# Kernel optimization log

Measured on AMD Instinct MI355X. Metric: run time of the kernel, lower is better.

## Reference

```python
import jax, jax.numpy as jnp
import numpy as np

B, N, E = 8, 4096, 8190
V, H, OUT = 256, 128, 128


def setup_inputs() -> dict:
    key = jax.random.key(0)
    ks = jax.random.split(key, 7)
    return {
        "type_ids": jax.random.randint(ks[0], (B, N), 0, V),
        "edges": jax.random.randint(ks[1], (B, E, 2), 0, N),
        "emb": jax.random.normal(ks[2], (V, H), jnp.float32) * 0.02,
        "w1": jax.random.normal(ks[3], (H, H), jnp.float32) * (1.0 / np.sqrt(H)),
        "b1": jax.random.normal(ks[4], (H,), jnp.float32) * 0.01,
        "w2": jax.random.normal(ks[5], (OUT, H), jnp.float32) * (1.0 / np.sqrt(H)),
        "b2": jax.random.normal(ks[6], (OUT,), jnp.float32) * 0.01,
    }


def reference(type_ids, edges, emb, w1, b1, w2, b2):
    # X: [B, N, H] embedded node types
    X = emb[type_ids]
    b_idx = jnp.broadcast_to(jnp.arange(type_ids.shape[0])[:, None], edges.shape[:2])
    # dense adjacency, set (not add) like torch adj[i, j] = 1.0; then + I
    adj = jnp.zeros((type_ids.shape[0], N, N), X.dtype)
    adj = adj.at[b_idx, edges[..., 0], edges[..., 1]].set(1.0)
    adj = adj + jnp.eye(N, dtype=X.dtype)
    # symmetric degree normalization: A = D^-1/2 (adj) D^-1/2
    deg = adj.sum(axis=-1)
    dis = jnp.maximum(deg, 1.0) ** -0.5  # deg.clamp(min=1.0) ** -0.5
    A = dis[:, :, None] * adj * dis[:, None, :]
    # two-layer GCN (torch Linear: x @ W.T + b)
    h = jax.nn.relu(jnp.einsum("bnm,bmh->bnh", A, X) @ w1.T + b1)
    z = jnp.einsum("bnm,bmh->bnh", A, h) @ w2.T + b2
    zbar = z.mean(axis=1)  # per-graph mean pool -> [B, OUT]
    # F.normalize(dim=-1), eps=1e-12
    norm = jnp.maximum(jnp.linalg.norm(zbar, axis=-1, keepdims=True), 1e-12)
    return zbar / norm
```

## Files before the change

kernel.cpp:

```cpp
#include <hip/hip_runtime.h>
#include <hip/hip_bf16.h>
#include <stdint.h>

#define BB 8
#define NN 4096
#define NE 8190
#define VV 256
#define HH 128
#define WPR2 128
#define MAXD 32
#define SLICES 32
#define RPW 4
#define NWAVE (BB * NN / RPW)


__device__ __forceinline__ int deco(int v) {
    unsigned u = (unsigned)v;
    return (int)(u - (u >= 0xAAAAAAAAu ? 0xAAAAAAAAu : 0u));
}

__global__ void k_scatter_embw1(const int* __restrict__ edges,
                                const float* __restrict__ emb,
                                const float* __restrict__ w1,
                                unsigned long long* __restrict__ bits,
                                int2* __restrict__ deg,
                                unsigned short* __restrict__ outl,
                                unsigned short* __restrict__ inl,
                                float* __restrict__ embw1) {
    int blk = blockIdx.x, t = threadIdx.x;
    if (blk < 256) {
        int idx = blk * 256 + t;
        if (idx >= BB * NE) return;
        int b = idx / NE;
        int src = edges[idx * 2 + 0];
        int dst = edges[idx * 2 + 1];
        int row = b * NN + src;
        unsigned long long m = 1ull << (2 * (dst & 31));
        unsigned long long old =
            atomicOr(&bits[(size_t)row * WPR2 + (dst >> 5)], m);
        if (!(old & m)) {
            int po = deco(atomicAdd(&deg[row].x, 1));
            if (po < MAXD) outl[(size_t)row * MAXD + po] = (unsigned short)dst;
            int col = b * NN + dst;
            int pi = deco(atomicAdd(&deg[col].y, 1));
            if (pi < MAXD) inl[(size_t)col * MAXD + pi] = (unsigned short)src;
        }
    } else {
        __shared__ float er[256];
        int v = (blk - 256) * 2 + (t >> 7);
        int o = t & 127;
        er[t] = emb[v * HH + o];
        __syncthreads();
        const float* erow = &er[(t >> 7) * HH];
        float acc = 0.f;
#pragma unroll 8
        for (int k = 0; k < HH; k++) acc += erow[k] * w1[o * HH + k];
        embw1[v * HH + o] = acc;
    }
}

__global__ void __launch_bounds__(256)
k_fused(const int* __restrict__ type_ids,
        const float* __restrict__ embw1,
        const int2* __restrict__ deg,
        const unsigned short* __restrict__ outl,
        const unsigned short* __restrict__ inl,
        const float* __restrict__ b1,
        float* __restrict__ p) {
    int lane = threadIdx.x & 63;
    int wid  = threadIdx.x >> 6;
    int gw   = blockIdx.x * 4 + wid;
    int base = gw * RPW;
    int b    = base >> 12;
    int e    = lane & 31;
    bool isOut = (lane < 32);
    float2 b1v = ((const float2*)b1)[lane];
    float2 psum; psum.x = 0.f; psum.y = 0.f;

    for (int r = 0; r < RPW; r++) {
        int row = base + r;
        int2 dg = deg[row];
        int odeg = deco(dg.x);
        int mo = min(odeg, MAXD);
        int mi = min(deco(dg.y), MAXD);
        int tid_i = type_ids[row];
        float dval = 0.f; int tval = 0;
        if (isOut ? (e < mo) : (e < mi)) {
            const unsigned short* lst = isOut ? outl : inl;
            int gj = b * NN + (int)lst[(size_t)row * MAXD + e];
            dval = rsqrtf((float)(deco(deg[gj].x) + 1));
            if (isOut) tval = type_ids[gj];
        }
        float s = dval;
#pragma unroll
        for (int off = 1; off <= 16; off <<= 1)
            s += __shfl_xor(s, off);
        float s_in = __shfl(s, 32);
        float dis_i = rsqrtf((float)(odeg + 1));
        float c_i = dis_i * (s_in + dis_i);
        float2 ev = ((const float2*)(embw1 + tid_i * HH))[lane];
        float2 acc; acc.x = dis_i * ev.x; acc.y = dis_i * ev.y;
        for (int q = 0; q < mo; q++) {
            float dj = __shfl(dval, q);
            int   tj = __shfl(tval, q);
            float2 evq = ((const float2*)(embw1 + tj * HH))[lane];
            acc.x += dj * evq.x;
            acc.y += dj * evq.y;
        }
        float h0 = fmaxf(dis_i * acc.x + b1v.x, 0.f);
        float h1 = fmaxf(dis_i * acc.y + b1v.y, 0.f);
        psum.x += c_i * h0;
        psum.y += c_i * h1;
    }
    int slice = gw & (SLICES - 1);
    float* pp = &p[((size_t)b * SLICES + slice) * HH + 2 * lane];
    atomicAdd(pp + 0, psum.x);
    atomicAdd(pp + 1, psum.y);
}

__global__ void k_final(const float* __restrict__ p,
                        const float* __restrict__ w2,
                        const float* __restrict__ b2,
                        float* __restrict__ out) {
    __shared__ float pl[HH];
    __shared__ float red[HH];
    int b = blockIdx.x, o = threadIdx.x;
    float accp = 0.f;
#pragma unroll 8
    for (int sct = 0; sct < SLICES; sct++)
        accp += p[((size_t)b * SLICES + sct) * HH + o];
    pl[o] = accp * (1.0f / (float)NN);
    __syncthreads();
    float acc = b2[o];
#pragma unroll 8
    for (int k = 0; k < HH; k++) acc += pl[k] * w2[o * HH + k];
    red[o] = acc * acc;
    __syncthreads();
    for (int stride = 64; stride > 0; stride >>= 1) {
        if (o < stride) red[o] += red[o + stride];
        __syncthreads();
    }
    float denom = fmaxf(sqrtf(red[0]), 1e-12f);
    out[b * HH + o] = acc / denom;
}

extern "C" void kernel_launch(void* const* d_in, const int* in_sizes, int n_in,
                              void* d_out, int out_size, void* d_ws, size_t ws_size,
                              hipStream_t stream) {
    const int*   type_ids = (const int*)d_in[0];
    const int*   edges    = (const int*)d_in[1];
    const float* emb      = (const float*)d_in[2];
    const float* w1       = (const float*)d_in[3];
    const float* b1       = (const float*)d_in[4];
    const float* w2       = (const float*)d_in[5];
    const float* b2       = (const float*)d_in[6];
    float* out = (float*)d_out;

    char* ws = (char*)d_ws;
    unsigned long long* bits = (unsigned long long*)ws;
    size_t off = (size_t)BB * NN * WPR2 * 8;
    int2* deg = (int2*)(ws + off);   off += (size_t)BB * NN * 8;
    float* p  = (float*)(ws + off);  off += (size_t)BB * SLICES * HH * 4;
    unsigned short* outl = (unsigned short*)(ws + off); off += (size_t)BB * NN * MAXD * 2;
    unsigned short* inl  = (unsigned short*)(ws + off); off += (size_t)BB * NN * MAXD * 2;
    float* embw1 = (float*)(ws + off);

    k_scatter_embw1<<<384, 256, 0, stream>>>(edges, emb, w1, bits, deg,
                                             outl, inl, embw1);
    k_fused<<<NWAVE / 4, 256, 0, stream>>>(type_ids, embw1, deg, outl, inl,
                                           b1, p);
    k_final<<<BB, HH, 0, stream>>>(p, w2, b2, out);
}
```

Before: 101.2 us.

## Vectorize loads, batch neighbor gathers, pack degree and type, widen final kernel

Vectorizes edge loads and the emb·W1 dot product with float4 reads. In the fused kernel, loads type ids and degrees for all four rows at once, issues every neighbor-list and degree gather before any compute so the loads overlap, and packs the truncated rsqrt degree and the type id into one int. Each neighbor then costs a single shuffle instead of two. The in-degree sum becomes a serial shuffle loop, and truncating the low mantissa bits slightly lowers precision. k_final uses 256 threads with split reductions, and launch bounds now request higher occupancy.

```diff
diff --git a/kernel.cpp b/kernel.cpp
--- a/kernel.cpp
+++ b/kernel.cpp
@@ -32,8 +32,9 @@
         int idx = blk * 256 + t;
         if (idx >= BB * NE) return;
         int b = idx / NE;
-        int src = edges[idx * 2 + 0];
-        int dst = edges[idx * 2 + 1];
+        int2 ed = ((const int2*)edges)[idx];
+        int src = ed.x;
+        int dst = ed.y;
         int row = b * NN + src;
         unsigned long long m = 1ull << (2 * (dst & 31));
         unsigned long long old =
@@ -51,15 +52,19 @@
         int o = t & 127;
         er[t] = emb[v * HH + o];
         __syncthreads();
-        const float* erow = &er[(t >> 7) * HH];
+        const float4* e4 = (const float4*)&er[(t >> 7) * HH];
+        const float4* w4 = (const float4*)(w1 + o * HH);
         float acc = 0.f;
-#pragma unroll 8
-        for (int k = 0; k < HH; k++) acc += erow[k] * w1[o * HH + k];
+#pragma unroll
+        for (int k = 0; k < HH / 4; k++) {
+            float4 a = e4[k], w = w4[k];
+            acc += a.x * w.x + a.y * w.y + a.z * w.z + a.w * w.w;
+        }
         embw1[v * HH + o] = acc;
     }
 }
 
-__global__ void __launch_bounds__(256)
+__global__ void __launch_bounds__(256, 8)
 k_fused(const int* __restrict__ type_ids,
         const float* __restrict__ embw1,
         const int2* __restrict__ deg,
@@ -72,38 +77,59 @@
     int gw   = blockIdx.x * 4 + wid;
     int base = gw * RPW;
     int b    = base >> 12;
+    int bN   = base & ~(NN - 1);
     int e    = lane & 31;
     bool isOut = (lane < 32);
     float2 b1v = ((const float2*)b1)[lane];
     float2 psum; psum.x = 0.f; psum.y = 0.f;
 
+    int4 t4 = *(const int4*)(type_ids + base);
+    int4 dA = *((const int4*)(deg + base));
+    int4 dB = *((const int4*)(deg + base) + 1);
+    int dgx[RPW] = {dA.x, dA.z, dB.x, dB.z};
+    int dgy[RPW] = {dA.y, dA.w, dB.y, dB.w};
+    int tii[RPW] = {t4.x, t4.y, t4.z, t4.w};
+
+    int nb[RPW];
+#pragma unroll
     for (int r = 0; r < RPW; r++) {
-        int row = base + r;
-        int2 dg = deg[row];
-        int odeg = deco(dg.x);
+        int m = isOut ? min(deco(dgx[r]), MAXD) : min(deco(dgy[r]), MAXD);
+        nb[r] = -1;
+        if (e < m) {
+            const unsigned short* lst = isOut ? outl : inl;
+            nb[r] = (int)lst[(size_t)(base + r) * MAXD + e];
+        }
+    }
+
+    int pk[RPW];
+#pragma unroll
+    for (int r = 0; r < RPW; r++) {
+        int v = 0;
+        if (nb[r] >= 0) {
+            int gj = bN + nb[r];
+            float dv = rsqrtf((float)(deco(deg[gj].x) + 1));
+            int tj = isOut ? type_ids[gj] : 0;
+            v = (__float_as_int(dv) & 0xFFFFFF00) | tj;
+        }
+        pk[r] = v;
+    }
+
+#pragma unroll
+    for (int r = 0; r < RPW; r++) {
+        int odeg = deco(dgx[r]);
         int mo = min(odeg, MAXD);
-        int mi = min(deco(dg.y), MAXD);
-        int tid_i = type_ids[row];
-        float dval = 0.f; int tval = 0;
-        if (isOut ? (e < mo) : (e < mi)) {
-            const unsigned short* lst = isOut ? outl : inl;
-            int gj = b * NN + (int)lst[(size_t)row * MAXD + e];
-            dval = rsqrtf((float)(deco(deg[gj].x) + 1));
-            if (isOut) tval = type_ids[gj];
-        }
-        float s = dval;
-#pragma unroll
-        for (int off = 1; off <= 16; off <<= 1)
-            s += __shfl_xor(s, off);
-        float s_in = __shfl(s, 32);
+        int mi = min(deco(dgy[r]), MAXD);
         float dis_i = rsqrtf((float)(odeg + 1));
+        float s_in = 0.f;
+        for (int q = 0; q < mi; q++)
+            s_in += __int_as_float(__shfl(pk[r], 32 + q));
         float c_i = dis_i * (s_in + dis_i);
-        float2 ev = ((const float2*)(embw1 + tid_i * HH))[lane];
+        float2 ev = ((const float2*)(embw1 + tii[r] * HH))[lane];
         float2 acc; acc.x = dis_i * ev.x; acc.y = dis_i * ev.y;
         for (int q = 0; q < mo; q++) {
-            float dj = __shfl(dval, q);
-            int   tj = __shfl(tval, q);
-            float2 evq = ((const float2*)(embw1 + tj * HH))[lane];
+            int pj = __shfl(pk[r], q);
+            float dj = __int_as_float(pj & 0xFFFFFF00);
+            float2 evq = ((const float2*)(embw1 + (pj & 255) * HH))[lane];
             acc.x += dj * evq.x;
             acc.y += dj * evq.y;
         }
@@ -112,36 +138,53 @@
         psum.x += c_i * h0;
         psum.y += c_i * h1;
     }
+
     int slice = gw & (SLICES - 1);
     float* pp = &p[((size_t)b * SLICES + slice) * HH + 2 * lane];
     atomicAdd(pp + 0, psum.x);
     atomicAdd(pp + 1, psum.y);
 }
 
-__global__ void k_final(const float* __restrict__ p,
-                        const float* __restrict__ w2,
-                        const float* __restrict__ b2,
-                        float* __restrict__ out) {
+__global__ void __launch_bounds__(256)
+k_final(const float* __restrict__ p,
+        const float* __restrict__ w2,
+        const float* __restrict__ b2,
+        float* __restrict__ out) {
     __shared__ float pl[HH];
-    __shared__ float red[HH];
-    int b = blockIdx.x, o = threadIdx.x;
+    __shared__ float red[256];
+    int bq = blockIdx.x, t = threadIdx.x;
+    int o = t & 127, hf = t >> 7;
+
     float accp = 0.f;
-#pragma unroll 8
-    for (int sct = 0; sct < SLICES; sct++)
-        accp += p[((size_t)b * SLICES + sct) * HH + o];
-    pl[o] = accp * (1.0f / (float)NN);
-    __syncthreads();
-    float acc = b2[o];
-#pragma unroll 8
-    for (int k = 0; k < HH; k++) acc += pl[k] * w2[o * HH + k];
-    red[o] = acc * acc;
-    __syncthreads();
-    for (int stride = 64; stride > 0; stride >>= 1) {
-        if (o < stride) red[o] += red[o + stride];
+    const float* pb = p + ((size_t)bq * SLICES + hf * (SLICES / 2)) * HH + o;
+#pragma unroll
+    for (int s = 0; s < SLICES / 2; s++) accp += pb[(size_t)s * HH];
+    red[t] = accp;
+    __syncthreads();
+    if (t < HH) pl[t] = (red[t] + red[t + HH]) * (1.0f / (float)NN);
+    __syncthreads();
+
+    float acc = 0.f;
+    const float* wrow = w2 + o * HH + hf * (HH / 2);
+    const float* plh  = pl + hf * (HH / 2);
+#pragma unroll
+    for (int k = 0; k < HH / 2 / 4; k++) {
+        float4 wv = ((const float4*)wrow)[k];
+        float4 pv = ((const float4*)plh)[k];
+        acc += pv.x * wv.x + pv.y * wv.y + pv.z * wv.z + pv.w * wv.w;
+    }
+    red[t] = acc;
+    __syncthreads();
+    float z = 0.f;
+    if (t < HH) z = red[t] + red[t + HH] + b2[t];
+    __syncthreads();
+    red[t] = z * z;
+    __syncthreads();
+    for (int stride = 64; stride >= 1; stride >>= 1) {
+        if (t < stride) red[t] += red[t + stride];
         __syncthreads();
     }
-    float denom = fmaxf(sqrtf(red[0]), 1e-12f);
-    out[b * HH + o] = acc / denom;
+    if (t < HH) out[bq * HH + t] = z / fmaxf(sqrtf(red[0]), 1e-12f);
 }
 
 extern "C" void kernel_launch(void* const* d_in, const int* in_sizes, int n_in,
@@ -169,5 +212,5 @@
                                              outl, inl, embw1);
     k_fused<<<NWAVE / 4, 256, 0, stream>>>(type_ids, embw1, deg, outl, inl,
                                            b1, p);
-    k_final<<<BB, HH, 0, stream>>>(p, w2, b2, out);
-}
+    k_final<<<BB, HH * 2, 0, stream>>>(p, w2, b2, out);
+}
```

Result: faster. 95.22 us (-5.9%).
